# Performance work log

Hardware: AMD Instinct MI355X
Metric: run time of the kernel (lower is better)

## Reference

```python
import jax, jax.numpy as jnp
import numpy as np

B, S, D, H = 4, 2048, 512, 8
HD = D // H  # 64


def setup_inputs() -> dict:
    key = jax.random.key(0)
    ks = jax.random.split(key, 7)
    scale = 1.0 / np.sqrt(D)
    return {
        "query": jax.random.normal(ks[0], (B, S, D), jnp.float32),
        "key": jax.random.normal(ks[1], (B, S, D), jnp.float32),
        "value": jax.random.normal(ks[2], (B, S, D), jnp.float32),
        # Only the `query` Linear and fc_out are actually used in the original forward
        "Wq": jax.random.uniform(ks[3], (D, D), jnp.float32, -scale, scale),
        "bq": jnp.zeros((D,), jnp.float32),
        "Wo": jax.random.uniform(ks[4], (D, D), jnp.float32, -scale, scale),
        "bo": jnp.zeros((D,), jnp.float32),
    }


def reference(query, key, value, Wq, bq, Wo, bo):
    # Faithful to source: Q, K, V all use the *query* projection (bug preserved)
    def proj(x):
        # [B,S,D] -> [B,H,S,HD]
        y = x @ Wq + bq
        return y.reshape(B, S, H, HD).transpose(0, 2, 1, 3)

    Q, K, V = proj(query), proj(key), proj(value)
    scores = jnp.einsum("bhqd,bhkd->bhqk", Q, K) / jnp.sqrt(jnp.float32(HD))
    attn = jax.nn.softmax(scores, axis=-1)
    x = jnp.einsum("bhqk,bhkd->bhqd", attn, V)
    x = x.transpose(0, 2, 1, 3).reshape(B, S, D)
    return x @ Wo + bo
```

## Files before the change

kernel.cpp:

```cpp
#include <hip/hip_runtime.h>
#include <math.h>

#define B_ 4
#define S_ 2048
#define D_ 512
#define H_ 8
#define HD_ 64
#define SZ_ (B_ * S_ * D_)
#define WSZ_ (D_ * D_)
#define BSH_ (B_ * S_ * H_)

#define QSCALE_ 0.18033688011112042f

typedef _Float16 v4h __attribute__((ext_vector_type(4)));
typedef _Float16 v8h __attribute__((ext_vector_type(8)));
typedef float    v4f __attribute__((ext_vector_type(4)));

__device__ __forceinline__ void gload16(const void* g, void* l) {
    __builtin_amdgcn_global_load_lds((__attribute__((address_space(1))) void*)g,
                                     (__attribute__((address_space(3))) void*)l,
                                     16, 0, 0);
}

__device__ __forceinline__ v8h pack8(v4f a, v4f b) {
    return __builtin_shufflevector(__builtin_convertvector(a, v4h),
                                   __builtin_convertvector(b, v4h),
                                   0, 1, 2, 3, 4, 5, 6, 7);
}

__global__ __launch_bounds__(256) void wtrans_kernel(const float* __restrict__ Wq,
                                                     const float* __restrict__ Wo,
                                                     _Float16* __restrict__ Wt) {
    __shared__ float Ts[64][132];
    const int kc = blockIdx.x, nt = blockIdx.y, mat = blockIdx.z;
    const float* W = mat ? Wo : Wq;
    const int k0 = kc * 64, n0 = nt * 128;
    const int t = threadIdx.x;
#pragma unroll
    for (int i = 0; i < 8; i++) {
        int s2 = t + i * 256;
        int kk = s2 >> 5, nc = (s2 & 31) * 4;
        *(float4*)&Ts[kk][nc] = *(const float4*)&W[(size_t)(k0 + kk) * 512 + n0 + nc];
    }
    __syncthreads();
    _Float16* blk = Wt + (((size_t)mat * 4 + nt) * 8 + kc) * 8192;
#pragma unroll
    for (int i = 0; i < 4; i++) {
        int s2 = t + i * 256;
        int r = s2 >> 3, s = s2 & 7;
        int kl = (s ^ (r & 7)) * 8;
        v8h p;
#pragma unroll
        for (int j = 0; j < 8; j++) p[j] = (_Float16)Ts[kl + j][r];
        *(v8h*)&blk[r * 64 + s * 8] = p;
    }
}

__global__ __launch_bounds__(256) void convert_f16(const float* __restrict__ q,
                                                   const float* __restrict__ k,
                                                   const float* __restrict__ v,
                                                   _Float16* __restrict__ Xh) {
    const int kc = blockIdx.x, mt = blockIdx.y, z = blockIdx.z;
    const float* X = (z == 0) ? q : ((z == 1) ? k : v);
    _Float16* blk = Xh + (size_t)z * SZ_ + ((size_t)mt * 8 + kc) * 8192;
    const int t = threadIdx.x;
#pragma unroll
    for (int i = 0; i < 4; i++) {
        int s2 = t + i * 256;
        int r = s2 >> 3, s = s2 & 7;
        const float* src = X + (size_t)(mt * 128 + r) * 512 + kc * 64 + s * 8;
        *(v8h*)&blk[r * 64 + ((s ^ (r & 7)) * 8)] =
            pack8(*(const v4f*)src, *(const v4f*)(src + 4));
    }
}

__global__ __launch_bounds__(256) void combine_kernel(const float* __restrict__ Op,
                                                      const float* __restrict__ lp,
                                                      _Float16* __restrict__ Ah) {
    const int kc = blockIdx.x, mt = blockIdx.y;
    _Float16* blk = Ah + ((size_t)mt * 8 + kc) * 8192;
    const int t = threadIdx.x;
#pragma unroll
    for (int i = 0; i < 4; i++) {
        int s2 = t + i * 256;
        int r = s2 >> 3, s = s2 & 7;
        size_t row = (size_t)mt * 128 + r;
        const float* p = Op + row * 512 + kc * 64 + s * 8;
        const float* p2 = p + SZ_;
        float linv = __builtin_amdgcn_rcpf(lp[row * 8 + kc] + lp[BSH_ + row * 8 + kc]);
        v4f sa = (*(const v4f*)p + *(const v4f*)p2) * linv;
        v4f sb = (*(const v4f*)(p + 4) + *(const v4f*)(p2 + 4)) * linv;
        *(v8h*)&blk[r * 64 + ((s ^ (r & 7)) * 8)] = pack8(sa, sb);
    }
}

__global__ __launch_bounds__(256) void proj_mfma(const _Float16* __restrict__ Xh,
                                                 const _Float16* __restrict__ Wt,
                                                 const float* __restrict__ bq,
                                                 _Float16* __restrict__ Qh,
                                                 _Float16* __restrict__ Kh,
                                                 _Float16* __restrict__ VT) {
    __shared__ __align__(16) _Float16 As[8192];
    __shared__ __align__(16) _Float16 Bs[8192];
    const int nt = blockIdx.x, mt = blockIdx.y, z = blockIdx.z;
    const int n0 = nt * 128, m0 = mt * 128;
    const int t = threadIdx.x, lane = t & 63, w = t >> 6;
    const int wm = w >> 1, wn = w & 1;
    const int quad = lane >> 4, l16 = lane & 15;

    const _Float16* Ab = Xh + (size_t)z * SZ_ + ((size_t)mt * 8) * 8192 + w * 512 + lane * 8;
    const _Float16* Bb = Wt + ((size_t)nt * 8) * 8192 + w * 512 + lane * 8;
    _Float16* Ad = As + w * 512;
    _Float16* Bd = Bs + w * 512;

    v4f acc[4][4];
#pragma unroll
    for (int mi = 0; mi < 4; mi++)
#pragma unroll
        for (int ni = 0; ni < 4; ni++) acc[mi][ni] = (v4f)0.f;

    for (int kc = 0; kc < 8; ++kc) {
        __syncthreads();
#pragma unroll
        for (int i = 0; i < 4; i++) {
            gload16(Ab + kc * 8192 + i * 2048, Ad + i * 2048);
            gload16(Bb + kc * 8192 + i * 2048, Bd + i * 2048);
        }
        __syncthreads();

#pragma unroll
        for (int ks = 0; ks < 2; ++ks) {
            const int sxx = (ks * 32 + quad * 8) ^ ((l16 & 7) * 8);
            v8h af[4], bf[4];
#pragma unroll
            for (int mi = 0; mi < 4; mi++)
                af[mi] = *(const v8h*)&As[(wm * 64 + mi * 16 + l16) * 64 + sxx];
#pragma unroll
            for (int ni = 0; ni < 4; ni++)
                bf[ni] = *(const v8h*)&Bs[(wn * 64 + ni * 16 + l16) * 64 + sxx];
#pragma unroll
            for (int mi = 0; mi < 4; mi++)
#pragma unroll
                for (int ni = 0; ni < 4; ni++)
                    acc[mi][ni] = __builtin_amdgcn_mfma_f32_16x16x32_f16(af[mi], bf[ni], acc[mi][ni], 0, 0, 0);
        }
    }

    if (z < 2) {
        _Float16* Y = z ? Kh : Qh;
        const float sc = z ? 1.f : QSCALE_;
#pragma unroll
        for (int mi = 0; mi < 4; mi++) {
            int mb = m0 + wm * 64 + mi * 16 + quad * 4;
#pragma unroll
            for (int ni = 0; ni < 4; ni++) {
                int n = n0 + wn * 64 + ni * 16 + l16;
                float bj = bq[n];
#pragma unroll
                for (int r = 0; r < 4; r++)
                    Y[(size_t)(mb + r) * 512 + n] = (_Float16)((acc[mi][ni][r] + bj) * sc);
            }
        }
    } else {
#pragma unroll
        for (int mi = 0; mi < 4; mi++) {
            int tile0 = (m0 & 2047) + wm * 64;
            int pos = tile0 + (mi >> 1) * 32 + quad * 8 + (mi & 1) * 4;
            int b = m0 >> 11;
#pragma unroll
            for (int ni = 0; ni < 4; ni++) {
                int n = n0 + wn * 64 + ni * 16 + l16;
                int h = n >> 6, dd = n & 63;
                float bj = bq[n];
                v4h pk;
#pragma unroll
                for (int r = 0; r < 4; r++) pk[r] = (_Float16)(acc[mi][ni][r] + bj);
                *(v4h*)&VT[(((size_t)b * H_ + h) * HD_ + dd) * S_ + pos] = pk;
            }
        }
    }
}

__global__ __launch_bounds__(256) void outproj_mfma(const _Float16* __restrict__ Ah,
                                                    const _Float16* __restrict__ Wt,
                                                    const float* __restrict__ bo,
                                                    float* __restrict__ out) {
    __shared__ __align__(16) _Float16 As[8192];
    __shared__ __align__(16) _Float16 Bs[8192];
    const int nt = blockIdx.x, mt = blockIdx.y;
    const int n0 = nt * 128, m0 = mt * 128;
    const int t = threadIdx.x, lane = t & 63, w = t >> 6;
    const int wm = w >> 1, wn = w & 1;
    const int quad = lane >> 4, l16 = lane & 15;

    const _Float16* Ab = Ah + ((size_t)mt * 8) * 8192 + w * 512 + lane * 8;
    const _Float16* Bb = Wt + (size_t)(4 + nt) * 8 * 8192 + w * 512 + lane * 8;
    _Float16* Ad = As + w * 512;
    _Float16* Bd = Bs + w * 512;

    v4f acc[4][4];
#pragma unroll
    for (int mi = 0; mi < 4; mi++)
#pragma unroll
        for (int ni = 0; ni < 4; ni++) acc[mi][ni] = (v4f)0.f;

    for (int kc = 0; kc < 8; ++kc) {
        __syncthreads();
#pragma unroll
        for (int i = 0; i < 4; i++) {
            gload16(Ab + kc * 8192 + i * 2048, Ad + i * 2048);
            gload16(Bb + kc * 8192 + i * 2048, Bd + i * 2048);
        }
        __syncthreads();

#pragma unroll
        for (int ks = 0; ks < 2; ++ks) {
            const int sxx = (ks * 32 + quad * 8) ^ ((l16 & 7) * 8);
            v8h af[4], bf[4];
#pragma unroll
            for (int mi = 0; mi < 4; mi++)
                af[mi] = *(const v8h*)&As[(wm * 64 + mi * 16 + l16) * 64 + sxx];
#pragma unroll
            for (int ni = 0; ni < 4; ni++)
                bf[ni] = *(const v8h*)&Bs[(wn * 64 + ni * 16 + l16) * 64 + sxx];
#pragma unroll
            for (int mi = 0; mi < 4; mi++)
#pragma unroll
                for (int ni = 0; ni < 4; ni++)
                    acc[mi][ni] = __builtin_amdgcn_mfma_f32_16x16x32_f16(af[mi], bf[ni], acc[mi][ni], 0, 0, 0);
        }
    }

#pragma unroll
    for (int mi = 0; mi < 4; mi++) {
        int mb = m0 + wm * 64 + mi * 16 + quad * 4;
#pragma unroll
        for (int ni = 0; ni < 4; ni++) {
            int n = n0 + wn * 64 + ni * 16 + l16;
            float bj = bo[n];
#pragma unroll
            for (int r = 0; r < 4; r++)
                out[(size_t)(mb + r) * 512 + n] = acc[mi][ni][r] + bj;
        }
    }
}

__global__ __launch_bounds__(256) void flash_attn_f16(const _Float16* __restrict__ Qh,
                                                      const _Float16* __restrict__ Kh,
                                                      const _Float16* __restrict__ VT,
                                                      float* __restrict__ Op,
                                                      float* __restrict__ lp) {
    __shared__ _Float16 Ks[128 * 72];
    __shared__ _Float16 Vs[64 * 136];

    const int t     = threadIdx.x;
    const int lane  = t & 63;
    const int w     = t >> 6;
    const int quad  = lane >> 4;
    const int l16   = lane & 15;
    const int q0    = blockIdx.x * 128;
    const int h     = blockIdx.y;
    const int b     = blockIdx.z >> 1;
    const int split = blockIdx.z & 1;

    const size_t base  = (size_t)b * S_ * D_ + (size_t)h * HD_;
    const size_t vbase = ((size_t)b * H_ + h) * HD_ * (size_t)S_;

    v8h qf[2][2];
#pragma unroll
    for (int nb = 0; nb < 2; nb++) {
        const _Float16* qrow = Qh + base + (size_t)(q0 + w * 32 + nb * 16 + l16) * D_;
        qf[nb][0] = *(const v8h*)(qrow + quad * 8);
        qf[nb][1] = *(const v8h*)(qrow + 32 + quad * 8);
    }

    v4f o[2][4];
#pragma unroll
    for (int nb = 0; nb < 2; nb++)
#pragma unroll
        for (int i = 0; i < 4; i++) o[nb][i] = (v4f)0.f;
    float l_lane[2] = {0.f, 0.f};

    const int kbeg = split * (S_ / 2);
    const int kend = kbeg + S_ / 2;

    v8h kv[4], vv[4];
#define LOADKV(kk)                                                             \
    do {                                                                       \
        _Pragma("unroll") for (int i = 0; i < 4; i++) {                        \
            int c = t + i * 256;                                               \
            kv[i] = *(const v8h*)(Kh + base + (size_t)((kk) + (c >> 3)) * D_ + (c & 7) * 8); \
            vv[i] = *(const v8h*)(VT + vbase + (size_t)(c >> 4) * S_ + (kk) + (c & 15) * 8); \
        }                                                                      \
    } while (0)

    LOADKV(kbeg);

    for (int kk0 = kbeg; kk0 < kend; kk0 += 128) {
        __syncthreads();
#pragma unroll
        for (int i = 0; i < 4; i++) {
            int c = t + i * 256;
            *(v8h*)&Ks[(c >> 3) * 72 + (c & 7) * 8] = kv[i];
            *(v8h*)&Vs[(c >> 4) * 136 + (c & 15) * 8] = vv[i];
        }
        __syncthreads();

        if (kk0 + 128 < kend) LOADKV(kk0 + 128);

#pragma unroll
        for (int hh = 0; hh < 2; hh++) {
            v4f sc[4][2];
#pragma unroll
            for (int mb = 0; mb < 4; mb++)
#pragma unroll
                for (int nb = 0; nb < 2; nb++) sc[mb][nb] = (v4f)0.f;
#pragma unroll
            for (int ks = 0; ks < 2; ks++) {
#pragma unroll
                for (int mb = 0; mb < 4; mb++) {
                    v8h ak = *(const v8h*)&Ks[(hh * 64 + mb * 16 + l16) * 72 + ks * 32 + quad * 8];
#pragma unroll
                    for (int nb = 0; nb < 2; nb++)
                        sc[mb][nb] = __builtin_amdgcn_mfma_f32_16x16x32_f16(ak, qf[nb][ks], sc[mb][nb], 0, 0, 0);
                }
            }

            v4h pf[4][2];
#pragma unroll
            for (int nb = 0; nb < 2; nb++) {
#pragma unroll
                for (int mb = 0; mb < 4; mb++) {
                    v4f pv;
#pragma unroll
                    for (int r = 0; r < 4; r++) pv[r] = __builtin_amdgcn_exp2f(sc[mb][nb][r]);
                    pf[mb][nb] = __builtin_convertvector(pv, v4h);
                    l_lane[nb] += (pv[0] + pv[1]) + (pv[2] + pv[3]);
                }
            }

#pragma unroll
            for (int p = 0; p < 2; p++) {
#pragma unroll
                for (int dblk = 0; dblk < 4; dblk++) {
                    v8h vf2 = *(const v8h*)&Vs[(dblk * 16 + l16) * 136 + hh * 64 + p * 32 + quad * 8];
                    v4h vlo = __builtin_shufflevector(vf2, vf2, 0, 1, 2, 3);
                    v4h vhi = __builtin_shufflevector(vf2, vf2, 4, 5, 6, 7);
#pragma unroll
                    for (int nb = 0; nb < 2; nb++) {
                        o[nb][dblk] = __builtin_amdgcn_mfma_f32_16x16x16f16(vlo, pf[2 * p][nb], o[nb][dblk], 0, 0, 0);
                        o[nb][dblk] = __builtin_amdgcn_mfma_f32_16x16x16f16(vhi, pf[2 * p + 1][nb], o[nb][dblk], 0, 0, 0);
                    }
                }
            }
        }
    }
#undef LOADKV

    float* Ops = Op + (size_t)split * SZ_;
#pragma unroll
    for (int nb = 0; nb < 2; nb++) {
        float rs = l_lane[nb];
        rs += __shfl_xor(rs, 16);
        rs += __shfl_xor(rs, 32);
        int qrow = q0 + w * 32 + nb * 16 + l16;
        if (quad == 0)
            lp[(size_t)split * BSH_ + ((size_t)b * S_ + qrow) * H_ + h] = rs;
        const size_t rbase = base + (size_t)qrow * D_;
#pragma unroll
        for (int dblk = 0; dblk < 4; dblk++)
            *(v4f*)&Ops[rbase + dblk * 16 + quad * 4] = o[nb][dblk];
    }
}

extern "C" void kernel_launch(void* const* d_in, const int* in_sizes, int n_in,
                              void* d_out, int out_size, void* d_ws, size_t ws_size,
                              hipStream_t stream) {
    const float* query = (const float*)d_in[0];
    const float* key   = (const float*)d_in[1];
    const float* value = (const float*)d_in[2];
    const float* Wq    = (const float*)d_in[3];
    const float* bq    = (const float*)d_in[4];
    const float* Wo    = (const float*)d_in[5];
    const float* bo    = (const float*)d_in[6];
    float* out = (float*)d_out;

    _Float16* ws = (_Float16*)d_ws;
    _Float16* Qh = ws;
    _Float16* Kh = ws + (size_t)SZ_;
    _Float16* VT = ws + 2 * (size_t)SZ_;
    _Float16* Wt = ws + 3 * (size_t)SZ_;
    _Float16* Xh = ws + 3 * (size_t)SZ_ + 2 * (size_t)WSZ_;
    float*    Op = (float*)Xh;
    float*    lp = Op + 2 * (size_t)SZ_;
    _Float16* Ah = Qh;

    wtrans_kernel<<<dim3(8, 4, 2), 256, 0, stream>>>(Wq, Wo, Wt);
    convert_f16<<<dim3(8, 64, 3), 256, 0, stream>>>(query, key, value, Xh);
    proj_mfma<<<dim3(4, 64, 3), 256, 0, stream>>>(Xh, Wt, bq, Qh, Kh, VT);
    flash_attn_f16<<<dim3(S_ / 128, H_, B_ * 2), 256, 0, stream>>>(Qh, Kh, VT, Op, lp);
    combine_kernel<<<dim3(8, 64), 256, 0, stream>>>(Op, lp, Ah);
    outproj_mfma<<<dim3(4, 64), 256, 0, stream>>>(Ah, Wt, bo, out);
}
```

Before: 202.0 us.

## Merge prep kernels, swizzle attention LDS tiles, use 16x16x32 MFMA for PV

```diff
diff --git a/kernel.cpp b/kernel.cpp
--- a/kernel.cpp
+++ b/kernel.cpp
@@ -28,14 +28,33 @@
                                    0, 1, 2, 3, 4, 5, 6, 7);
 }
 
-__global__ __launch_bounds__(256) void wtrans_kernel(const float* __restrict__ Wq,
-                                                     const float* __restrict__ Wo,
-                                                     _Float16* __restrict__ Wt) {
+__global__ __launch_bounds__(256) void prep_f16(const float* __restrict__ q,
+                                                const float* __restrict__ k,
+                                                const float* __restrict__ v,
+                                                const float* __restrict__ Wq,
+                                                const float* __restrict__ Wo,
+                                                _Float16* __restrict__ Xh,
+                                                _Float16* __restrict__ Wt) {
+    const int kc = blockIdx.x, my = blockIdx.y, z = blockIdx.z;
+    const int t = threadIdx.x;
+    if (z < 3) {
+        const float* X = (z == 0) ? q : ((z == 1) ? k : v);
+        _Float16* blk = Xh + (size_t)z * SZ_ + ((size_t)my * 8 + kc) * 8192;
+#pragma unroll
+        for (int i = 0; i < 4; i++) {
+            int s2 = t + i * 256;
+            int r = s2 >> 3, s = s2 & 7;
+            const float* src = X + (size_t)(my * 128 + r) * 512 + kc * 64 + s * 8;
+            *(v8h*)&blk[r * 64 + ((s ^ (r & 7)) * 8)] =
+                pack8(*(const v4f*)src, *(const v4f*)(src + 4));
+        }
+        return;
+    }
+    if (my >= 8) return;
+    const int mat = my >> 2, nt = my & 3;
     __shared__ float Ts[64][132];
-    const int kc = blockIdx.x, nt = blockIdx.y, mat = blockIdx.z;
     const float* W = mat ? Wo : Wq;
     const int k0 = kc * 64, n0 = nt * 128;
-    const int t = threadIdx.x;
 #pragma unroll
     for (int i = 0; i < 8; i++) {
         int s2 = t + i * 256;
@@ -53,24 +72,6 @@
 #pragma unroll
         for (int j = 0; j < 8; j++) p[j] = (_Float16)Ts[kl + j][r];
         *(v8h*)&blk[r * 64 + s * 8] = p;
-    }
-}
-
-__global__ __launch_bounds__(256) void convert_f16(const float* __restrict__ q,
-                                                   const float* __restrict__ k,
-                                                   const float* __restrict__ v,
-                                                   _Float16* __restrict__ Xh) {
-    const int kc = blockIdx.x, mt = blockIdx.y, z = blockIdx.z;
-    const float* X = (z == 0) ? q : ((z == 1) ? k : v);
-    _Float16* blk = Xh + (size_t)z * SZ_ + ((size_t)mt * 8 + kc) * 8192;
-    const int t = threadIdx.x;
-#pragma unroll
-    for (int i = 0; i < 4; i++) {
-        int s2 = t + i * 256;
-        int r = s2 >> 3, s = s2 & 7;
-        const float* src = X + (size_t)(mt * 128 + r) * 512 + kc * 64 + s * 8;
-        *(v8h*)&blk[r * 64 + ((s ^ (r & 7)) * 8)] =
-            pack8(*(const v4f*)src, *(const v4f*)(src + 4));
     }
 }
 
@@ -250,8 +251,8 @@
                                                       const _Float16* __restrict__ VT,
                                                       float* __restrict__ Op,
                                                       float* __restrict__ lp) {
-    __shared__ _Float16 Ks[128 * 72];
-    __shared__ _Float16 Vs[64 * 136];
+    __shared__ _Float16 Ks[128 * 64];
+    __shared__ _Float16 Vs[64 * 128];
 
     const int t     = threadIdx.x;
     const int lane  = t & 63;
@@ -301,8 +302,10 @@
 #pragma unroll
         for (int i = 0; i < 4; i++) {
             int c = t + i * 256;
-            *(v8h*)&Ks[(c >> 3) * 72 + (c & 7) * 8] = kv[i];
-            *(v8h*)&Vs[(c >> 4) * 136 + (c & 15) * 8] = vv[i];
+            int rk = c >> 3, sk = c & 7;
+            *(v8h*)&Ks[rk * 64 + ((sk ^ (rk & 7)) * 8)] = kv[i];
+            int rv = c >> 4, sv = c & 15;
+            *(v8h*)&Vs[rv * 128 + ((sv ^ (rv & 7)) * 8)] = vv[i];
         }
         __syncthreads();
 
@@ -319,7 +322,8 @@
             for (int ks = 0; ks < 2; ks++) {
 #pragma unroll
                 for (int mb = 0; mb < 4; mb++) {
-                    v8h ak = *(const v8h*)&Ks[(hh * 64 + mb * 16 + l16) * 72 + ks * 32 + quad * 8];
+                    v8h ak = *(const v8h*)&Ks[(hh * 64 + mb * 16 + l16) * 64 +
+                                              (((ks * 4 + quad) ^ (l16 & 7)) * 8)];
 #pragma unroll
                     for (int nb = 0; nb < 2; nb++)
                         sc[mb][nb] = __builtin_amdgcn_mfma_f32_16x16x32_f16(ak, qf[nb][ks], sc[mb][nb], 0, 0, 0);
@@ -343,13 +347,13 @@
             for (int p = 0; p < 2; p++) {
 #pragma unroll
                 for (int dblk = 0; dblk < 4; dblk++) {
-                    v8h vf2 = *(const v8h*)&Vs[(dblk * 16 + l16) * 136 + hh * 64 + p * 32 + quad * 8];
-                    v4h vlo = __builtin_shufflevector(vf2, vf2, 0, 1, 2, 3);
-                    v4h vhi = __builtin_shufflevector(vf2, vf2, 4, 5, 6, 7);
+                    v8h vf2 = *(const v8h*)&Vs[(dblk * 16 + l16) * 128 +
+                                               (((hh * 8 + p * 4 + quad) ^ (l16 & 7)) * 8)];
 #pragma unroll
                     for (int nb = 0; nb < 2; nb++) {
-                        o[nb][dblk] = __builtin_amdgcn_mfma_f32_16x16x16f16(vlo, pf[2 * p][nb], o[nb][dblk], 0, 0, 0);
-                        o[nb][dblk] = __builtin_amdgcn_mfma_f32_16x16x16f16(vhi, pf[2 * p + 1][nb], o[nb][dblk], 0, 0, 0);
+                        v8h pf8 = __builtin_shufflevector(pf[2 * p][nb], pf[2 * p + 1][nb],
+                                                          0, 1, 2, 3, 4, 5, 6, 7);
+                        o[nb][dblk] = __builtin_amdgcn_mfma_f32_16x16x32_f16(vf2, pf8, o[nb][dblk], 0, 0, 0);
                     }
                 }
             }
@@ -395,8 +399,7 @@
     float*    lp = Op + 2 * (size_t)SZ_;
     _Float16* Ah = Qh;
 
-    wtrans_kernel<<<dim3(8, 4, 2), 256, 0, stream>>>(Wq, Wo, Wt);
-    convert_f16<<<dim3(8, 64, 3), 256, 0, stream>>>(query, key, value, Xh);
+    prep_f16<<<dim3(8, 64, 4), 256, 0, stream>>>(query, key, value, Wq, Wo, Xh, Wt);
     proj_mfma<<<dim3(4, 64, 3), 256, 0, stream>>>(Xh, Wt, bq, Qh, Kh, VT);
     flash_attn_f16<<<dim3(S_ / 128, H_, B_ * 2), 256, 0, stream>>>(Qh, Kh, VT, Op, lp);
     combine_kernel<<<dim3(8, 64), 256, 0, stream>>>(Op, lp, Ah);
```

New measurement: 202.5 us. No clear change (+0.3%).
